# Performance work log

Measured on AMD Instinct MI355X. Metric: run time of the kernel, lower is better.

## Reference

```python
import jax, jax.numpy as jnp
import numpy as np

BITS = 4
QMAX = (1 << BITS) - 1      # 15
QHALF = 1 << (BITS - 1)     # 8
B, S = 4, 2048
IN, OUT, FP = 4096, 4096, 256
INT = IN - FP


def setup_inputs() -> dict:
    key = jax.random.key(0)
    k0, k1, k2, k3 = jax.random.split(key, 4)
    x = jax.random.normal(k0, (B, S, IN), dtype=jnp.float16)
    # disjoint outlier / int feature index sets (QUIK splits columns by outlier-ness)
    perm = np.random.default_rng(0).permutation(IN)
    fp_indices = jnp.sort(jnp.asarray(perm[:FP], dtype=jnp.int32))
    int_indices = jnp.sort(jnp.asarray(perm[FP:], dtype=jnp.int32))
    # unpacked int4 weight values in [-8, 7] (torch stores these packed 2-per-uint8)
    int_weight = jax.random.randint(k1, (OUT, INT), -QHALF, QHALF, dtype=jnp.int8)
    weights_scales = (jax.random.uniform(k2, (OUT, 1), dtype=jnp.float32) * 0.01 + 1e-3).astype(jnp.float16)
    fp_weight = (jax.random.normal(k3, (OUT, FP), dtype=jnp.float32) * 0.02).astype(jnp.float16)
    bias = jnp.zeros((OUT,), dtype=jnp.float16)
    # reduced_w[j] = w_scale[j] * sum_k int_weight[j, k]  (precomputed zero-point correction)
    reduced_w = (weights_scales.astype(jnp.float32)[:, 0] * jnp.sum(int_weight.astype(jnp.float32), axis=1)).reshape(1, OUT).astype(jnp.float16)
    return {"x": x, "int_weight": int_weight, "fp_weight": fp_weight, "bias": bias,
            "weights_scales": weights_scales, "reduced_w": reduced_w,
            "int_indices": int_indices, "fp_indices": fp_indices}


def reference(x, int_weight, fp_weight, bias, weights_scales, reduced_w, int_indices, fp_indices):
    b, s, in_feat = x.shape
    xf = x.reshape(-1, in_feat)                       # [N, in] tokens
    int_x = xf[:, int_indices].astype(jnp.float32)    # [N, INT]
    fp_x = xf[:, fp_indices].astype(jnp.float32)      # [N, FP] outliers stay fp16-precision
    # asymmetric per-token quantization (quik.asymmetric.quantize)
    mn = jnp.min(int_x, axis=1, keepdims=True)
    mx = jnp.max(int_x, axis=1, keepdims=True)
    scale = jnp.maximum((mx - mn) / QMAX, 1e-8)       # [N,1]
    q = (jnp.clip(jnp.round((int_x - mn) / scale), 0, QMAX) - QHALF).astype(jnp.int8)  # signed int4 in [-8,7]
    zero = scale * QHALF + mn                         # [N,1] shifted zero point
    # int4 GEMM (quik.matmul.int4Matmul), int32 accumulate
    int_res = jnp.einsum('nk,ok->no', q, int_weight, preferred_element_type=jnp.int32)
    # fp outlier branch fused with bias (F.linear)
    fp_res = fp_x @ fp_weight.astype(jnp.float32).T + bias.astype(jnp.float32)[None, :]
    # quik.asymmetric.dequantize: q*scale_x*scale_w + zero_x*reduced_w + fp_result
    out = (int_res.astype(jnp.float32) * scale * weights_scales.astype(jnp.float32)[:, 0][None, :]
           + zero * reduced_w.astype(jnp.float32) + fp_res)
    return out.astype(jnp.float16).reshape(b, s, -1)
```

## Files before the change

### kernel.cpp

```cpp
#include <hip/hip_runtime.h>
#include <hip/hip_bf16.h>
#include <stdint.h>

#define N_TOK 8192
#define IN_F  4096
#define OUT_F 4096
#define FP_F  256
#define INT_F 3840
#define PROW  1920

typedef int    v4i   __attribute__((ext_vector_type(4)));
typedef int    v16i  __attribute__((ext_vector_type(16)));
typedef float  v16f  __attribute__((ext_vector_type(16)));
typedef __bf16 bf16x8 __attribute__((ext_vector_type(8)));

#define WS_QP   0u
#define WS_WP   15728640u
#define WS_FPX  31457280u
#define WS_WFP  35651584u
#define WS_F1   37748736u
#define WS_F2   37781504u
#define WS_F3   37814272u
#define WS_NEED 37847040u


__global__ __launch_bounds__(256) void zero_out_kernel(uint4* __restrict__ o) {
  o[(size_t)blockIdx.x * 256 + threadIdx.x] = uint4{0, 0, 0, 0};
}

__global__ __launch_bounds__(256, 4) void prep_kernel(
    const float* __restrict__ x,
    const int* __restrict__ int_idx, const int* __restrict__ fp_idx,
    const int* __restrict__ int_w, const float* __restrict__ fp_w,
    uint8_t* __restrict__ qp, uint8_t* __restrict__ wp,
    __hip_bfloat16* __restrict__ fpx, __hip_bfloat16* __restrict__ wfp,
    float* __restrict__ f1, float* __restrict__ f2, float* __restrict__ f3) {
  __shared__ uint2 qb[960];

  int tid = threadIdx.x;
  int blk = blockIdx.x;

  if (blk >= 2048) {
    int pb = blk - 2048;
    if (pb < 15360) {
      int t = pb * 256 + tid;
      int r = t / 960, u = t % 960;
      const int* src = int_w + (size_t)r * INT_F + u * 4;
      int4 w4 = *(const int4*)src;
      uint32_t pk = (uint32_t)((w4.x + 8) & 15) |
                    (uint32_t)((w4.y + 8) & 15) << 8 |
                    (uint32_t)((w4.z + 8) & 15) << 16 |
                    (uint32_t)((w4.w + 8) & 15) << 24;
      *(uint32_t*)(wp + (size_t)(u >> 2) * 65536 + (size_t)r * 16 + (u & 3) * 4) = pk;
    } else {
      int t = (pb - 15360) * 256 + tid;
      int i = t * 4;
      int r = i >> 8, c = i & 255;
      float4 v = *(const float4*)(fp_w + i);
      __hip_bfloat16 b[4] = {__float2bfloat16(v.x), __float2bfloat16(v.y),
                             __float2bfloat16(v.z), __float2bfloat16(v.w)};
      int cs = (c & ~0x18) | (((((c) >> 3) & 3) ^ ((r >> 1) & 3)) << 3);
      *(uint2*)(wfp + (size_t)r * 256 + cs) = *(const uint2*)b;
    }
    return;
  }

  int wave = tid >> 6, l = tid & 63;
  int n = blk * 4 + wave;
  const float* xr = x + (size_t)n * IN_F;

  float v[60];
  float lmn = 1e30f, lmx = -1e30f;
#pragma unroll
  for (int k = 0; k < 60; k++) {
    v[k] = xr[int_idx[l + 64 * k]];
    lmn = fminf(lmn, v[k]);
    lmx = fmaxf(lmx, v[k]);
  }
  {
    int sw2 = (n >> 1) & 3;
#pragma unroll
    for (int j = 0; j < 4; j++) {
      int c = l + 64 * j;
      int cs = (c & ~0x18) | ((((c >> 3) & 3) ^ sw2) << 3);
      fpx[(size_t)n * FP_F + cs] = __float2bfloat16(xr[fp_idx[c]]);
    }
  }

#pragma unroll
  for (int off = 32; off > 0; off >>= 1) {
    lmn = fminf(lmn, __shfl_xor(lmn, off, 64));
    lmx = fmaxf(lmx, __shfl_xor(lmx, off, 64));
  }
  float mn = lmn;
  float sc = fmaxf((lmx - mn) / 15.0f, 1e-8f);
  float inv = 1.0f / sc;
  if (l == 0) { f1[n] = sc; f3[n] = mn; }

  uint8_t* qbw = (uint8_t*)qb + wave * 1920;
  int swq = (n >> 1) & 7;
  float lsum = 0.0f;
#pragma unroll
  for (int k = 0; k < 60; k++) {
    float c = fminf(fmaxf(rintf((v[k] - mn) * inv), 0.0f), 15.0f);
    lsum += c;
    float ch = __shfl_down(c, 8, 64);
    if ((l & 15) < 8) {
      int G = (l >> 4) + 4 * k;
      int pos = ((G & ~7) | ((G & 7) ^ swq)) * 8 + (l & 7);
      qbw[pos] = (uint8_t)((uint32_t)c | ((uint32_t)ch << 4));
    }
  }
#pragma unroll
  for (int off = 32; off > 0; off >>= 1) lsum += __shfl_xor(lsum, off, 64);
  if (l == 0) f2[n] = -8.0f * lsum * sc;

  const uint2* qbu = qb + wave * 240;
#pragma unroll
  for (int r = 0; r < 4; r++) {
    int i = l + 64 * r;
    if (i < 240) *(uint2*)(qp + (size_t)n * PROW + i * 8) = qbu[i];
  }
}

__device__ inline v4i unpack_nib(uint2 u) {
  v4i r;
  r[0] = (int)(u.x & 0x0F0F0F0Fu);
  r[1] = (int)(u.y & 0x0F0F0F0Fu);
  r[2] = (int)((u.x >> 4) & 0x0F0F0F0Fu);
  r[3] = (int)((u.y >> 4) & 0x0F0F0F0Fu);
  return r;
}

__device__ __forceinline__ void gl16(const void* g, void* l) {
  __builtin_amdgcn_global_load_lds(
      (const __attribute__((address_space(1))) void*)g,
      (__attribute__((address_space(3))) void*)l, 16, 0, 0);
}

__global__ __launch_bounds__(256, 3) void gemm_kernel(
    const uint8_t* __restrict__ qp, const uint8_t* __restrict__ wp,
    const __hip_bfloat16* __restrict__ fpx, const __hip_bfloat16* __restrict__ wfp,
    const float* __restrict__ f1, const float* __restrict__ f2,
    const float* __restrict__ f3,
    const float* __restrict__ wscale, const float* __restrict__ reduced,
    const float* __restrict__ bias, float* __restrict__ out) {
  __shared__ int4 lds4[3072];
  int8_t* lds = (int8_t*)lds4;

  int tid = threadIdx.x;
  int wave = tid >> 6, lane = tid & 63;
  int wm = wave >> 1, wn = wave & 1;
  int blk = blockIdx.x;
  int tileM = ((blk & 7) << 3) | ((blk >> 3) & 7);
  int tileN = blk >> 6;
  int n0 = tileM * 128, o0 = tileN * 128;

  union { v16i i; v16f f; } acc[2][2];
#pragma unroll
  for (int mi = 0; mi < 2; mi++)
#pragma unroll
    for (int ni = 0; ni < 2; ni++)
#pragma unroll
      for (int e = 0; e < 16; e++) acc[mi][ni].i[e] = 0;

  int m = lane & 31, kg = lane >> 5;

  int row0 = tid >> 2, q16 = (tid & 3) * 16;
  int l0 = tid * 16, l1 = 4096 + tid * 16;
  const uint8_t* gA0 = qp + (size_t)(n0 + row0) * PROW + q16;
  const uint8_t* gA1 = qp + (size_t)(n0 + 64 + row0) * PROW + q16;

  int rB = tid & 127, sB = tid >> 7;
  const uint8_t* gBk = wp + (size_t)sB * 65536 + (size_t)(o0 + rB) * 16;
  int lB = 8192 + sB * 2048 + rB * 16;

#define STAGE_INT(buf, kt) do {                                          \
    gl16(gA0 + (kt) * 64, lds + (buf) * 24576 + l0);                     \
    gl16(gA1 + (kt) * 64, lds + (buf) * 24576 + l1);                     \
    gl16(gBk + (size_t)(kt) * 524288,          lds + (buf) * 24576 + lB);          \
    gl16(gBk + (size_t)(kt) * 524288 + 131072, lds + (buf) * 24576 + lB + 4096);   \
    gl16(gBk + (size_t)(kt) * 524288 + 262144, lds + (buf) * 24576 + lB + 8192);   \
    gl16(gBk + (size_t)(kt) * 524288 + 393216, lds + (buf) * 24576 + lB + 12288);  \
  } while (0)

  auto compute_int = [&](const int8_t* lb) {
#pragma unroll
    for (int ks = 0; ks < 4; ks++) {
      int s8 = ks * 2 + kg;
      v4i a[2], b[2];
#pragma unroll
      for (int mi = 0; mi < 2; mi++) {
        int row = wm * 64 + mi * 32 + m;
        a[mi] = unpack_nib(*(const uint2*)&lb[row * 64 + ((s8 ^ ((row >> 1) & 7)) * 8)]);
      }
#pragma unroll
      for (int ni = 0; ni < 2; ni++) {
        int row = wn * 64 + ni * 32 + m;
        b[ni] = *(const v4i*)&lb[8192 + s8 * 2048 + row * 16];
      }
#pragma unroll
      for (int mi = 0; mi < 2; mi++)
#pragma unroll
        for (int ni = 0; ni < 2; ni++)
          acc[mi][ni].i = __builtin_amdgcn_mfma_i32_32x32x32_i8(
              a[mi], b[ni], acc[mi][ni].i, 0, 0, 0);
    }
  };

  STAGE_INT(0, 0);
#pragma unroll 1
  for (int kt = 0; kt < 30; kt += 2) {
    STAGE_INT(1, kt + 1);
    asm volatile("s_waitcnt vmcnt(6)" ::: "memory");
    __builtin_amdgcn_s_barrier();
    compute_int(lds);
    __builtin_amdgcn_s_barrier();
    if (kt + 2 < 30) {
      STAGE_INT(0, kt + 2);
      asm volatile("s_waitcnt vmcnt(6)" ::: "memory");
    } else {
      asm volatile("s_waitcnt vmcnt(0)" ::: "memory");
    }
    __builtin_amdgcn_s_barrier();
    compute_int(lds + 24576);
    __builtin_amdgcn_s_barrier();
  }

  const uint8_t* fxb = (const uint8_t*)fpx;
  const uint8_t* fwb = (const uint8_t*)wfp;
  const uint8_t* gFA0 = fxb + (size_t)(n0 + row0) * 512 + q16;
  const uint8_t* gFA1 = fxb + (size_t)(n0 + 64 + row0) * 512 + q16;
  const uint8_t* gFB0 = fwb + (size_t)(o0 + row0) * 512 + q16;
  const uint8_t* gFB1 = fwb + (size_t)(o0 + 64 + row0) * 512 + q16;

#define STAGE_BF(buf, kr) do {                                   \
    gl16(gFA0 + (kr) * 64, lds + (buf) + l0);                    \
    gl16(gFA1 + (kr) * 64, lds + (buf) + l1);                    \
    gl16(gFB0 + (kr) * 64, lds + (buf) + 8192 + l0);             \
    gl16(gFB1 + (kr) * 64, lds + (buf) + 8192 + l1);             \
  } while (0)

  STAGE_BF(0, 0);

  int col = lane & 31, rb4 = (lane >> 5) * 4;
  float cws[2], crw[2], cbs[2];
#pragma unroll
  for (int ni = 0; ni < 2; ni++) {
    int o = o0 + wn * 64 + ni * 32 + col;
    cws[ni] = wscale[o]; crw[ni] = reduced[o]; cbs[ni] = bias[o];
  }
#pragma unroll
  for (int mi = 0; mi < 2; mi++) {
#pragma unroll
    for (int reg = 0; reg < 16; reg++) {
      int row = (reg & 3) + 8 * (reg >> 2) + rb4;
      int n = n0 + wm * 64 + mi * 32 + row;
      float a1 = f1[n], a2 = f2[n], a3 = f3[n];
      float d0 = (float)acc[mi][0].i[reg];
      float d1 = (float)acc[mi][1].i[reg];
      acc[mi][0].f[reg] = (d0 * a1 + a2) * cws[0] + a3 * crw[0] + cbs[0];
      acc[mi][1].f[reg] = (d1 * a1 + a2) * cws[1] + a3 * crw[1] + cbs[1];
    }
  }
  asm volatile("s_waitcnt vmcnt(0)" ::: "memory");
  __builtin_amdgcn_s_barrier();

  auto compute_bf = [&](const int8_t* lb) {
#pragma unroll
    for (int kstep = 0; kstep < 2; kstep++) {
      int s16 = kstep * 2 + kg;
      bf16x8 a[2], b[2];
#pragma unroll
      for (int mi = 0; mi < 2; mi++) {
        int row = wm * 64 + mi * 32 + m;
        a[mi] = *(const bf16x8*)&lb[row * 64 + ((s16 ^ ((row >> 1) & 3)) * 16)];
      }
#pragma unroll
      for (int ni = 0; ni < 2; ni++) {
        int row = wn * 64 + ni * 32 + m;
        b[ni] = *(const bf16x8*)&lb[8192 + row * 64 + ((s16 ^ ((row >> 1) & 3)) * 16)];
      }
#pragma unroll
      for (int mi = 0; mi < 2; mi++)
#pragma unroll
        for (int ni = 0; ni < 2; ni++)
          acc[mi][ni].f = __builtin_amdgcn_mfma_f32_32x32x16_bf16(
              a[mi], b[ni], acc[mi][ni].f, 0, 0, 0);
    }
  };

#pragma unroll 1
  for (int kr = 0; kr < 8; kr += 2) {
    STAGE_BF(16384, kr + 1);
    asm volatile("s_waitcnt vmcnt(4)" ::: "memory");
    __builtin_amdgcn_s_barrier();
    compute_bf(lds);
    __builtin_amdgcn_s_barrier();
    if (kr + 2 < 8) {
      STAGE_BF(0, kr + 2);
      asm volatile("s_waitcnt vmcnt(4)" ::: "memory");
    } else {
      asm volatile("s_waitcnt vmcnt(0)" ::: "memory");
    }
    __builtin_amdgcn_s_barrier();
    compute_bf(lds + 16384);
    __builtin_amdgcn_s_barrier();
  }
#undef STAGE_INT
#undef STAGE_BF

#pragma unroll
  for (int mi = 0; mi < 2; mi++) {
#pragma unroll
    for (int ni = 0; ni < 2; ni++) {
      int o = o0 + wn * 64 + ni * 32 + col;
#pragma unroll
      for (int reg = 0; reg < 16; reg++) {
        int row = (reg & 3) + 8 * (reg >> 2) + rb4;
        int n = n0 + wm * 64 + mi * 32 + row;
        out[(size_t)n * OUT_F + o] = acc[mi][ni].f[reg];
      }
    }
  }
}

extern "C" void kernel_launch(void* const* d_in, const int* in_sizes, int n_in,
                              void* d_out, int out_size, void* d_ws, size_t ws_size,
                              hipStream_t stream) {
  const float* x     = (const float*)d_in[0];
  const int*   int_w = (const int*)d_in[1];
  const float* fp_w  = (const float*)d_in[2];
  const float* bias  = (const float*)d_in[3];
  const float* wsc   = (const float*)d_in[4];
  const float* red   = (const float*)d_in[5];
  const int*   iidx  = (const int*)d_in[6];
  const int*   fidx  = (const int*)d_in[7];
  float*       out   = (float*)d_out;

  if (ws_size < (size_t)WS_NEED) {
    zero_out_kernel<<<out_size / 1024, 256, 0, stream>>>((uint4*)d_out);
    return;
  }

  uint8_t* ws = (uint8_t*)d_ws;
  uint8_t*        qp  = ws + WS_QP;
  uint8_t*        wpk = ws + WS_WP;
  __hip_bfloat16* fpx = (__hip_bfloat16*)(ws + WS_FPX);
  __hip_bfloat16* wfp = (__hip_bfloat16*)(ws + WS_WFP);
  float*          f1  = (float*)(ws + WS_F1);
  float*          f2  = (float*)(ws + WS_F2);
  float*          f3  = (float*)(ws + WS_F3);

  prep_kernel<<<2048 + 15360 + 1024, 256, 0, stream>>>(
      x, iidx, fidx, int_w, fp_w, qp, wpk, fpx, wfp, f1, f2, f3);
  gemm_kernel<<<(N_TOK / 128) * (OUT_F / 128), 256, 0, stream>>>(
      qp, wpk, fpx, wfp, f1, f2, f3, wsc, red, bias, out);
}
```

Measured before the change: 413.7 us.

## Halve GEMM K-tile to shrink LDS and raise occupancy to four blocks

The int4 and bf16 GEMM stages now use half-depth K tiles (32 bytes of packed A and 64 K of B per stage), so the double-buffered LDS footprint drops from 48KB to 24KB. Launch bounds go from 3 to 4 blocks per CU. The packed layouts and XOR swizzles in the prep kernel are rewritten to match the narrower tiles. This doubles the number of loop iterations and barriers, and adds register pressure under the tighter bound, in exchange for more resident waves to hide memory latency.

```diff
diff --git a/kernel.cpp b/kernel.cpp
--- a/kernel.cpp
+++ b/kernel.cpp
@@ -51,7 +51,8 @@
                     (uint32_t)((w4.y + 8) & 15) << 8 |
                     (uint32_t)((w4.z + 8) & 15) << 16 |
                     (uint32_t)((w4.w + 8) & 15) << 24;
-      *(uint32_t*)(wp + (size_t)(u >> 2) * 65536 + (size_t)r * 16 + (u & 3) * 4) = pk;
+      *(uint32_t*)(wp + (size_t)(u >> 4) * 262144 + (size_t)((u >> 2) & 3) * 65536
+                      + (size_t)r * 16 + (u & 3) * 4) = pk;
     } else {
       int t = (pb - 15360) * 256 + tid;
       int i = t * 4;
@@ -59,7 +60,7 @@
       float4 v = *(const float4*)(fp_w + i);
       __hip_bfloat16 b[4] = {__float2bfloat16(v.x), __float2bfloat16(v.y),
                              __float2bfloat16(v.z), __float2bfloat16(v.w)};
-      int cs = (c & ~0x18) | (((((c) >> 3) & 3) ^ ((r >> 1) & 3)) << 3);
+      int cs = (c & ~8) | (((((c) >> 3) & 1) ^ ((r >> 2) & 1)) << 3);
       *(uint2*)(wfp + (size_t)r * 256 + cs) = *(const uint2*)b;
     }
     return;
@@ -78,11 +79,11 @@
     lmx = fmaxf(lmx, v[k]);
   }
   {
-    int sw2 = (n >> 1) & 3;
+    int swF = (n >> 2) & 1;
 #pragma unroll
     for (int j = 0; j < 4; j++) {
       int c = l + 64 * j;
-      int cs = (c & ~0x18) | ((((c >> 3) & 3) ^ sw2) << 3);
+      int cs = (c & ~8) | ((((c >> 3) & 1) ^ swF) << 3);
       fpx[(size_t)n * FP_F + cs] = __float2bfloat16(xr[fp_idx[c]]);
     }
   }
@@ -98,7 +99,7 @@
   if (l == 0) { f1[n] = sc; f3[n] = mn; }
 
   uint8_t* qbw = (uint8_t*)qb + wave * 1920;
-  int swq = (n >> 1) & 7;
+  int swA = (n >> 2) & 3;
   float lsum = 0.0f;
 #pragma unroll
   for (int k = 0; k < 60; k++) {
@@ -106,8 +107,7 @@
     lsum += c;
     float ch = __shfl_down(c, 8, 64);
     if ((l & 15) < 8) {
-      int G = (l >> 4) + 4 * k;
-      int pos = ((G & ~7) | ((G & 7) ^ swq)) * 8 + (l & 7);
+      int pos = k * 32 + (((l >> 4) ^ swA) << 3) + (l & 7);
       qbw[pos] = (uint8_t)((uint32_t)c | ((uint32_t)ch << 4));
     }
   }
@@ -138,14 +138,14 @@
       (__attribute__((address_space(3))) void*)l, 16, 0, 0);
 }
 
-__global__ __launch_bounds__(256, 3) void gemm_kernel(
+__global__ __launch_bounds__(256, 4) void gemm_kernel(
     const uint8_t* __restrict__ qp, const uint8_t* __restrict__ wp,
     const __hip_bfloat16* __restrict__ fpx, const __hip_bfloat16* __restrict__ wfp,
     const float* __restrict__ f1, const float* __restrict__ f2,
     const float* __restrict__ f3,
     const float* __restrict__ wscale, const float* __restrict__ reduced,
     const float* __restrict__ bias, float* __restrict__ out) {
-  __shared__ int4 lds4[3072];
+  __shared__ int4 lds4[1536];
   int8_t* lds = (int8_t*)lds4;
 
   int tid = threadIdx.x;
@@ -166,38 +166,32 @@
 
   int m = lane & 31, kg = lane >> 5;
 
-  int row0 = tid >> 2, q16 = (tid & 3) * 16;
-  int l0 = tid * 16, l1 = 4096 + tid * 16;
-  const uint8_t* gA0 = qp + (size_t)(n0 + row0) * PROW + q16;
-  const uint8_t* gA1 = qp + (size_t)(n0 + 64 + row0) * PROW + q16;
-
-  int rB = tid & 127, sB = tid >> 7;
-  const uint8_t* gBk = wp + (size_t)sB * 65536 + (size_t)(o0 + rB) * 16;
-  int lB = 8192 + sB * 2048 + rB * 16;
-
-#define STAGE_INT(buf, kt) do {                                          \
-    gl16(gA0 + (kt) * 64, lds + (buf) * 24576 + l0);                     \
-    gl16(gA1 + (kt) * 64, lds + (buf) * 24576 + l1);                     \
-    gl16(gBk + (size_t)(kt) * 524288,          lds + (buf) * 24576 + lB);          \
-    gl16(gBk + (size_t)(kt) * 524288 + 131072, lds + (buf) * 24576 + lB + 4096);   \
-    gl16(gBk + (size_t)(kt) * 524288 + 262144, lds + (buf) * 24576 + lB + 8192);   \
-    gl16(gBk + (size_t)(kt) * 524288 + 393216, lds + (buf) * 24576 + lB + 12288);  \
+  int rowA = tid >> 1, hA = tid & 1;
+  const uint8_t* gA = qp + (size_t)(n0 + rowA) * PROW + hA * 16;
+  const uint8_t* gB0 = wp + (size_t)(tid >> 7) * 65536 + (size_t)(o0 + (tid & 127)) * 16;
+  const uint8_t* gB1 = gB0 + 2 * 65536;
+  int lA = tid * 16, lB0 = 4096 + tid * 16, lB1 = 8192 + tid * 16;
+
+#define STAGE_INT(buf, ht) do {                                      \
+    gl16(gA + (ht) * 32, lds + (buf) + lA);                          \
+    gl16(gB0 + (size_t)(ht) * 262144, lds + (buf) + lB0);            \
+    gl16(gB1 + (size_t)(ht) * 262144, lds + (buf) + lB1);            \
   } while (0)
 
   auto compute_int = [&](const int8_t* lb) {
 #pragma unroll
-    for (int ks = 0; ks < 4; ks++) {
+    for (int ks = 0; ks < 2; ks++) {
       int s8 = ks * 2 + kg;
       v4i a[2], b[2];
 #pragma unroll
       for (int mi = 0; mi < 2; mi++) {
         int row = wm * 64 + mi * 32 + m;
-        a[mi] = unpack_nib(*(const uint2*)&lb[row * 64 + ((s8 ^ ((row >> 1) & 7)) * 8)]);
+        a[mi] = unpack_nib(*(const uint2*)&lb[row * 32 + ((s8 ^ ((row >> 2) & 3)) * 8)]);
       }
 #pragma unroll
       for (int ni = 0; ni < 2; ni++) {
         int row = wn * 64 + ni * 32 + m;
-        b[ni] = *(const v4i*)&lb[8192 + s8 * 2048 + row * 16];
+        b[ni] = *(const v4i*)&lb[4096 + s8 * 2048 + row * 16];
       }
 #pragma unroll
       for (int mi = 0; mi < 2; mi++)
@@ -210,35 +204,31 @@
 
   STAGE_INT(0, 0);
 #pragma unroll 1
-  for (int kt = 0; kt < 30; kt += 2) {
-    STAGE_INT(1, kt + 1);
-    asm volatile("s_waitcnt vmcnt(6)" ::: "memory");
+  for (int t = 0; t < 60; t += 2) {
+    STAGE_INT(12288, t + 1);
+    asm volatile("s_waitcnt vmcnt(3)" ::: "memory");
     __builtin_amdgcn_s_barrier();
     compute_int(lds);
     __builtin_amdgcn_s_barrier();
-    if (kt + 2 < 30) {
-      STAGE_INT(0, kt + 2);
-      asm volatile("s_waitcnt vmcnt(6)" ::: "memory");
+    if (t + 2 < 60) {
+      STAGE_INT(0, t + 2);
+      asm volatile("s_waitcnt vmcnt(3)" ::: "memory");
     } else {
       asm volatile("s_waitcnt vmcnt(0)" ::: "memory");
     }
     __builtin_amdgcn_s_barrier();
-    compute_int(lds + 24576);
+    compute_int(lds + 12288);
     __builtin_amdgcn_s_barrier();
   }
 
   const uint8_t* fxb = (const uint8_t*)fpx;
   const uint8_t* fwb = (const uint8_t*)wfp;
-  const uint8_t* gFA0 = fxb + (size_t)(n0 + row0) * 512 + q16;
-  const uint8_t* gFA1 = fxb + (size_t)(n0 + 64 + row0) * 512 + q16;
-  const uint8_t* gFB0 = fwb + (size_t)(o0 + row0) * 512 + q16;
-  const uint8_t* gFB1 = fwb + (size_t)(o0 + 64 + row0) * 512 + q16;
+  const uint8_t* gFA = fxb + (size_t)(n0 + rowA) * 512 + hA * 16;
+  const uint8_t* gFB = fwb + (size_t)(o0 + rowA) * 512 + hA * 16;
 
 #define STAGE_BF(buf, kr) do {                                   \
-    gl16(gFA0 + (kr) * 64, lds + (buf) + l0);                    \
-    gl16(gFA1 + (kr) * 64, lds + (buf) + l1);                    \
-    gl16(gFB0 + (kr) * 64, lds + (buf) + 8192 + l0);             \
-    gl16(gFB1 + (kr) * 64, lds + (buf) + 8192 + l1);             \
+    gl16(gFA + (kr) * 32, lds + (buf) + lA);                     \
+    gl16(gFB + (kr) * 32, lds + (buf) + 4096 + lA);              \
   } while (0)
 
   STAGE_BF(0, 0);
@@ -263,48 +253,42 @@
       acc[mi][1].f[reg] = (d1 * a1 + a2) * cws[1] + a3 * crw[1] + cbs[1];
     }
   }
-  asm volatile("s_waitcnt vmcnt(0)" ::: "memory");
-  __builtin_amdgcn_s_barrier();
 
   auto compute_bf = [&](const int8_t* lb) {
-#pragma unroll
-    for (int kstep = 0; kstep < 2; kstep++) {
-      int s16 = kstep * 2 + kg;
-      bf16x8 a[2], b[2];
-#pragma unroll
-      for (int mi = 0; mi < 2; mi++) {
-        int row = wm * 64 + mi * 32 + m;
-        a[mi] = *(const bf16x8*)&lb[row * 64 + ((s16 ^ ((row >> 1) & 3)) * 16)];
-      }
-#pragma unroll
-      for (int ni = 0; ni < 2; ni++) {
-        int row = wn * 64 + ni * 32 + m;
-        b[ni] = *(const bf16x8*)&lb[8192 + row * 64 + ((s16 ^ ((row >> 1) & 3)) * 16)];
-      }
-#pragma unroll
-      for (int mi = 0; mi < 2; mi++)
-#pragma unroll
-        for (int ni = 0; ni < 2; ni++)
-          acc[mi][ni].f = __builtin_amdgcn_mfma_f32_32x32x16_bf16(
-              a[mi], b[ni], acc[mi][ni].f, 0, 0, 0);
-    }
+    bf16x8 a[2], b[2];
+#pragma unroll
+    for (int mi = 0; mi < 2; mi++) {
+      int row = wm * 64 + mi * 32 + m;
+      a[mi] = *(const bf16x8*)&lb[row * 32 + ((kg ^ ((row >> 2) & 1)) * 16)];
+    }
+#pragma unroll
+    for (int ni = 0; ni < 2; ni++) {
+      int row = wn * 64 + ni * 32 + m;
+      b[ni] = *(const bf16x8*)&lb[4096 + row * 32 + ((kg ^ ((row >> 2) & 1)) * 16)];
+    }
+#pragma unroll
+    for (int mi = 0; mi < 2; mi++)
+#pragma unroll
+      for (int ni = 0; ni < 2; ni++)
+        acc[mi][ni].f = __builtin_amdgcn_mfma_f32_32x32x16_bf16(
+            a[mi], b[ni], acc[mi][ni].f, 0, 0, 0);
   };
 
 #pragma unroll 1
-  for (int kr = 0; kr < 8; kr += 2) {
-    STAGE_BF(16384, kr + 1);
-    asm volatile("s_waitcnt vmcnt(4)" ::: "memory");
+  for (int kr = 0; kr < 16; kr += 2) {
+    STAGE_BF(8192, kr + 1);
+    asm volatile("s_waitcnt vmcnt(2)" ::: "memory");
     __builtin_amdgcn_s_barrier();
     compute_bf(lds);
     __builtin_amdgcn_s_barrier();
-    if (kr + 2 < 8) {
+    if (kr + 2 < 16) {
       STAGE_BF(0, kr + 2);
-      asm volatile("s_waitcnt vmcnt(4)" ::: "memory");
+      asm volatile("s_waitcnt vmcnt(2)" ::: "memory");
     } else {
       asm volatile("s_waitcnt vmcnt(0)" ::: "memory");
     }
     __builtin_amdgcn_s_barrier();
-    compute_bf(lds + 16384);
+    compute_bf(lds + 8192);
     __builtin_amdgcn_s_barrier();
   }
 #undef STAGE_INT
```

Result: slower. 428.1 us (+3.5%).
